# Kernel tuning notes

Hardware: AMD Instinct MI355X
Metric: run time of the kernel (lower is better)

Reference implementation:

```python
import jax, jax.numpy as jnp
import numpy as np

IN_C = 31
OUT_C = 31
GRID = 5          # grid_size
K = 3             # spline_order
NUM_BASIS = GRID + K                  # 8 B-spline basis functions
COEF_LEN = IN_C * OUT_C * NUM_BASIS   # 7688
UW_LEN = IN_C * OUT_C                 # 961 (univariate_weight)
RW_LEN = IN_C * OUT_C                 # 961 (residual_weight)
PNUM = COEF_LEN + UW_LEN + RW_LEN     # 9610 = kan_params_num


def _ext_grid():
    # uniform grid on grid_range=(-1,1), extended by K knots on each side
    h = 2.0 / GRID
    return jnp.arange(-K, GRID + K + 1, dtype=jnp.float32) * h - 1.0  # (GRID+2K+1,)


def bspline_basis(x):
    # x: (N, IN_C) -> (N, IN_C, NUM_BASIS) via Cox-de Boor recursion
    grid = _ext_grid()
    xx = x[..., None]
    b = ((xx >= grid[:-1]) & (xx < grid[1:])).astype(x.dtype)
    for p in range(1, K + 1):
        left = (xx - grid[: -(p + 1)]) / (grid[p:-1] - grid[: -(p + 1)]) * b[..., :-1]
        right = (grid[p + 1:] - xx) / (grid[p + 1:] - grid[1:-p]) * b[..., 1:]
        b = left + right
    return b


def setup_inputs() -> dict:
    key = jax.random.key(0)
    k1, k2, k3 = jax.random.split(key, 3)
    x = jax.random.normal(k1, (1, IN_C, 128, 128), jnp.float32)
    # HyperspectralGeneratorLayer: per-pixel (1x1 conv) map in_channels -> kan_params_num
    gen_w = jax.random.normal(k2, (PNUM, IN_C), jnp.float32) * 0.02
    gen_b = jax.random.normal(k3, (PNUM,), jnp.float32) * 0.02
    return {"x": x, "gen_w": gen_w, "gen_b": gen_b}


def reference(x, gen_w, gen_b):
    B, C, H, W = x.shape
    xf = x.transpose(0, 2, 3, 1).reshape(B * H * W, C)      # (N, 31)
    # generator: per-pixel KAN parameter vector (N, 9610)
    w = xf @ gen_w.T + gen_b
    coef = w[:, :COEF_LEN].reshape(-1, IN_C, OUT_C, NUM_BASIS)
    uw = w[:, COEF_LEN:COEF_LEN + UW_LEN].reshape(-1, IN_C, OUT_C)
    rw = w[:, COEF_LEN + UW_LEN:].reshape(-1, IN_C, OUT_C)
    # per-pixel KAN: phi_ij(x_i) = uw_ij * spline_ij(x_i) + rw_ij * silu(x_i); y_j = sum_i phi_ij
    basis = bspline_basis(xf)                               # (N, 31, 8)
    spline = jnp.einsum('nik,niok->nio', basis, coef)       # (N, 31, 31)
    y = jnp.einsum('nio,nio->no', spline, uw) \
        + jnp.einsum('ni,nio->no', jax.nn.silu(xf), rw)     # (N, 31)
    return y.reshape(B, H, W, OUT_C).transpose(0, 3, 1, 2)
```

## Files before the change

kernel.cpp:

```cpp
#include <hip/hip_runtime.h>
#include <hip/hip_bf16.h>
#include <math.h>

#define IN_C 31
#define OUT_C 31
#define NPIX 16384
#define UW_OFF 7688
#define RW_OFF 8649
#define PART_OFF (640 * 1024)
#define CHUNK_BYTES 20480

typedef __attribute__((ext_vector_type(8))) _Float16 f16x8;
typedef __attribute__((ext_vector_type(4))) float f32x4;

__device__ inline short f2h(float f) {
    union { _Float16 h; short s; } cv;
    cv.h = (_Float16)f;
    return cv.s;
}

__global__ __launch_bounds__(64) void kan_prep_kernel(
    const float* __restrict__ gw, const float* __restrict__ gb,
    unsigned short* __restrict__ ws)
{
    const int blk = blockIdx.x;
    const int i   = blk / 20;
    const int ch  = blk % 20;
    const int l   = threadIdx.x;
    const int col = l & 15;
    const int krow = l >> 4;
    const int o = (ch & 1) * 16 + col;

    int p;
    if (ch < 16)      p = (i * 31 + o) * 8 + (ch >> 1);
    else if (ch < 18) p = UW_OFF + i * 31 + o;
    else              p = RW_OFF + i * 31 + o;

    short v8[8];
#pragma unroll
    for (int j = 0; j < 8; ++j) {
        const int c = krow * 8 + j;
        float v = 0.f;
        if (o < OUT_C) v = (c < IN_C) ? gw[p * 31 + c] : gb[p];
        v8[j] = f2h(v);
    }
    *(f16x8*)&ws[(blk * 64 + l) * 8] = *(f16x8*)v8;
}

__device__ __forceinline__ void stage_i(const unsigned char* wsrc,
                                        unsigned char* ldst, int t) {
#pragma unroll
    for (int k = 0; k < 2; ++k) {
        const int off = (k * 512 + t) * 16;
        __builtin_amdgcn_global_load_lds(
            (const __attribute__((address_space(1))) unsigned int*)(wsrc + off),
            (__attribute__((address_space(3))) unsigned int*)(ldst + off),
            16, 0, 0);
    }
    if (t < 256) {
        const int off = (1024 + t) * 16;
        __builtin_amdgcn_global_load_lds(
            (const __attribute__((address_space(1))) unsigned int*)(wsrc + off),
            (__attribute__((address_space(3))) unsigned int*)(ldst + off),
            16, 0, 0);
    }
}

__device__ __forceinline__ void compute2(
    int iA, const unsigned char* wbA, bool hasB, int iB, const unsigned char* wbB,
    const float* __restrict__ x, int pr0, f16x8 xv8f, f32x4 Y[2], int l)
{
    const float xa = x[iA * NPIX + pr0];
    const float xb = hasB ? x[iB * NPIX + pr0] : 0.f;

    _Float16 basA[8], basB[8];
    f16x8 arwA, arwB;
#pragma unroll
    for (int s = 0; s < 2; ++s) {
        const float xv = (s == 0) ? xa : xb;
        const float tb = (xv + 2.2f) * 2.5f;
        const float jf = floorf(tb);
        const float u  = tb - jf;
        const int  jj  = (int)jf;
        const float u2 = u * u, u3 = u2 * u;
        const float b0v = u3 * (1.f / 6.f);
        const float b1v = (-3.f * u3 + 3.f * u2 + 3.f * u + 1.f) * (1.f / 6.f);
        const float b2v = (3.f * u3 - 6.f * u2 + 4.f) * (1.f / 6.f);
        const float omu = 1.f - u;
        const float b3v = omu * omu * omu * (1.f / 6.f);
#pragma unroll
        for (int m = 0; m < 8; ++m) {
            const int d = jj - m;
            const float bv = (d == 0) ? b0v : (d == 1) ? b1v : (d == 2) ? b2v
                           : (d == 3) ? b3v : 0.f;
            if (s == 0) basA[m] = (_Float16)bv; else basB[m] = (_Float16)bv;
        }
        const float sil = xv / (1.f + __expf(-xv));
        if (s == 0) arwA = xv8f * (_Float16)sil;
        else        arwB = xv8f * (_Float16)sil;
    }

    f32x4 SPA[2], UWA[2], SPB[2], UWB[2];
#pragma unroll
    for (int nt = 0; nt < 2; ++nt) {
        SPA[nt] = (f32x4){0.f, 0.f, 0.f, 0.f};
        UWA[nt] = (f32x4){0.f, 0.f, 0.f, 0.f};
        SPB[nt] = (f32x4){0.f, 0.f, 0.f, 0.f};
        UWB[nt] = (f32x4){0.f, 0.f, 0.f, 0.f};
    }

#pragma unroll
    for (int p = 0; p < 10; ++p) {
        const f16x8 a0 = *(const f16x8*)(wbA + ((p * 2 + 0) * 64 + l) * 16);
        const f16x8 a1 = *(const f16x8*)(wbA + ((p * 2 + 1) * 64 + l) * 16);
        const f16x8 c0 = *(const f16x8*)(wbB + ((p * 2 + 0) * 64 + l) * 16);
        const f16x8 c1 = *(const f16x8*)(wbB + ((p * 2 + 1) * 64 + l) * 16);
        if (p < 8) {
            const f16x8 afA = xv8f * basA[p];
            SPA[0] = __builtin_amdgcn_mfma_f32_16x16x32_f16(afA, a0, SPA[0], 0, 0, 0);
            SPA[1] = __builtin_amdgcn_mfma_f32_16x16x32_f16(afA, a1, SPA[1], 0, 0, 0);
            if (hasB) {
                const f16x8 afB = xv8f * basB[p];
                SPB[0] = __builtin_amdgcn_mfma_f32_16x16x32_f16(afB, c0, SPB[0], 0, 0, 0);
                SPB[1] = __builtin_amdgcn_mfma_f32_16x16x32_f16(afB, c1, SPB[1], 0, 0, 0);
            }
        } else if (p == 8) {
            UWA[0] = __builtin_amdgcn_mfma_f32_16x16x32_f16(xv8f, a0, UWA[0], 0, 0, 0);
            UWA[1] = __builtin_amdgcn_mfma_f32_16x16x32_f16(xv8f, a1, UWA[1], 0, 0, 0);
            if (hasB) {
                UWB[0] = __builtin_amdgcn_mfma_f32_16x16x32_f16(xv8f, c0, UWB[0], 0, 0, 0);
                UWB[1] = __builtin_amdgcn_mfma_f32_16x16x32_f16(xv8f, c1, UWB[1], 0, 0, 0);
            }
        } else {
            Y[0] = __builtin_amdgcn_mfma_f32_16x16x32_f16(arwA, a0, Y[0], 0, 0, 0);
            Y[1] = __builtin_amdgcn_mfma_f32_16x16x32_f16(arwA, a1, Y[1], 0, 0, 0);
            if (hasB) {
                Y[0] = __builtin_amdgcn_mfma_f32_16x16x32_f16(arwB, c0, Y[0], 0, 0, 0);
                Y[1] = __builtin_amdgcn_mfma_f32_16x16x32_f16(arwB, c1, Y[1], 0, 0, 0);
            }
        }
    }

#pragma unroll
    for (int nt = 0; nt < 2; ++nt)
#pragma unroll
        for (int r = 0; r < 4; ++r) {
            Y[nt][r] = fmaf(UWA[nt][r], SPA[nt][r], Y[nt][r]);
            if (hasB) Y[nt][r] = fmaf(UWB[nt][r], SPB[nt][r], Y[nt][r]);
        }
}

__global__ __launch_bounds__(512) void kan_mfma14_kernel(
    const float* __restrict__ x,
    const unsigned char* __restrict__ wsw,
    float* __restrict__ parts,
    float* __restrict__ out,
    int nsplit)
{
    const int t = threadIdx.x;
    const int l = t & 63;
    const int w = t >> 6;
    const int pix0 = blockIdx.x * 128;
    const int csize = (IN_C + nsplit - 1) / nsplit;
    const int ibase = blockIdx.y * csize;
    const int iend = min(ibase + csize, IN_C);

    __shared__ __align__(16) unsigned char bufs[2][CHUNK_BYTES];

    const int n0 = w * 16;
    const int pr0 = pix0 + n0 + (l & 15);

    stage_i(wsw + (size_t)ibase * CHUNK_BYTES, bufs[0], t);
    stage_i(wsw + (size_t)(ibase + 1) * CHUNK_BYTES, bufs[1], t);

    f16x8 xv8f;
    {
        const int cb = (l >> 4) * 8;
#pragma unroll
        for (int j = 0; j < 8; ++j) {
            const int c = cb + j;
            const float v = (c < IN_C) ? x[c * NPIX + pr0] : 1.0f;
            xv8f[j] = (_Float16)v;
        }
    }

    f32x4 Y[2];
    Y[0] = (f32x4){0.f, 0.f, 0.f, 0.f};
    Y[1] = (f32x4){0.f, 0.f, 0.f, 0.f};

    __syncthreads();

    compute2(ibase, bufs[0], true, ibase + 1, bufs[1], x, pr0, xv8f, Y, l);

    __syncthreads();

    const bool has3 = (ibase + 3) < iend;
    stage_i(wsw + (size_t)(ibase + 2) * CHUNK_BYTES, bufs[0], t);
    if (has3)
        stage_i(wsw + (size_t)(ibase + 3) * CHUNK_BYTES, bufs[1], t);

    __syncthreads();

    compute2(ibase + 2, bufs[0], has3, ibase + 3, bufs[1], x, pr0, xv8f, Y, l);

    __syncthreads();
    float* yb = (float*)bufs;
#pragma unroll
    for (int nt = 0; nt < 2; ++nt)
#pragma unroll
        for (int r = 0; r < 4; ++r) {
            const int p = n0 + (l >> 4) * 4 + r;
            const int o = nt * 16 + (l & 15);
            if (o < OUT_C) yb[p * 33 + o] = Y[nt][r];
        }
    __syncthreads();

    float* dst = (blockIdx.y == 0) ? out
               : (parts + (size_t)(blockIdx.y - 1) * OUT_C * NPIX);
    for (int idx = t; idx < 128 * OUT_C; idx += 512) {
        const int n = idx & 127, o = idx >> 7;
        dst[o * NPIX + pix0 + n] = yb[n * 33 + o];
    }
}

__global__ __launch_bounds__(256) void kan_combine_kernel(
    float* __restrict__ out, const float* __restrict__ parts, int npart)
{
    const int e = blockIdx.x * 256 + threadIdx.x;
    const int nv = (OUT_C * NPIX) / 4;
    if (e < nv) {
        f32x4 a = ((const f32x4*)out)[e];
        for (int j = 0; j < npart; ++j)
            a += ((const f32x4*)parts)[e + (size_t)j * nv];
        ((f32x4*)out)[e] = a;
    }
}

extern "C" void kernel_launch(void* const* d_in, const int* in_sizes, int n_in,
                              void* d_out, int out_size, void* d_ws, size_t ws_size,
                              hipStream_t stream) {
    const float* x  = (const float*)d_in[0];
    const float* gw = (const float*)d_in[1];
    const float* gb = (const float*)d_in[2];
    float* out = (float*)d_out;
    unsigned short* ws = (unsigned short*)d_ws;
    float* parts = (float*)((char*)d_ws + PART_OFF);

    const size_t part_bytes = (size_t)OUT_C * NPIX * 4;
    int nsplit = 8;
    if (ws_size < PART_OFF + 7 * part_bytes) nsplit = 4;
    if (ws_size < PART_OFF + 3 * part_bytes) nsplit = 2;

    hipLaunchKernelGGL(kan_prep_kernel, dim3(620), dim3(64), 0, stream, gw, gb, ws);
    hipLaunchKernelGGL(kan_mfma14_kernel, dim3(NPIX / 128, nsplit), dim3(512), 0, stream,
                       x, (const unsigned char*)d_ws, parts, out, nsplit);
    const int nv = (OUT_C * NPIX) / 4;
    hipLaunchKernelGGL(kan_combine_kernel, dim3((nv + 255) / 256), dim3(256), 0, stream,
                       out, parts, nsplit - 1);
}
```

Measured before the change: 41.99 us.

## Swap MFMA operands and apply spline basis weights after matmul in fp32

Instead of scaling the x vector by each basis value before each MFMA, the kernel now computes the plain generator product for each basis slot (weights as A, x as B) and applies the basis and silu weights in fp32 with FMA on the outputs. It also replaces the fixed two-pass structure with a generic loop over input-channel pairs, adding bounds checks. Each MFMA now starts from a zero accumulator followed by VALU FMAs, which removes the per-step f16 vector scaling but adds VALU work and serial dependencies. The output transpose indexing is changed to match the swapped operand layout.

```diff
diff --git a/kernel.cpp b/kernel.cpp
--- a/kernel.cpp
+++ b/kernel.cpp
@@ -66,91 +66,64 @@
     }
 }
 
-__device__ __forceinline__ void compute2(
-    int iA, const unsigned char* wbA, bool hasB, int iB, const unsigned char* wbB,
-    const float* __restrict__ x, int pr0, f16x8 xv8f, f32x4 Y[2], int l)
-{
-    const float xa = x[iA * NPIX + pr0];
-    const float xb = hasB ? x[iB * NPIX + pr0] : 0.f;
-
-    _Float16 basA[8], basB[8];
-    f16x8 arwA, arwB;
-#pragma unroll
-    for (int s = 0; s < 2; ++s) {
-        const float xv = (s == 0) ? xa : xb;
-        const float tb = (xv + 2.2f) * 2.5f;
-        const float jf = floorf(tb);
-        const float u  = tb - jf;
-        const int  jj  = (int)jf;
-        const float u2 = u * u, u3 = u2 * u;
-        const float b0v = u3 * (1.f / 6.f);
-        const float b1v = (-3.f * u3 + 3.f * u2 + 3.f * u + 1.f) * (1.f / 6.f);
-        const float b2v = (3.f * u3 - 6.f * u2 + 4.f) * (1.f / 6.f);
-        const float omu = 1.f - u;
-        const float b3v = omu * omu * omu * (1.f / 6.f);
-#pragma unroll
-        for (int m = 0; m < 8; ++m) {
-            const int d = jj - m;
-            const float bv = (d == 0) ? b0v : (d == 1) ? b1v : (d == 2) ? b2v
-                           : (d == 3) ? b3v : 0.f;
-            if (s == 0) basA[m] = (_Float16)bv; else basB[m] = (_Float16)bv;
-        }
-        const float sil = xv / (1.f + __expf(-xv));
-        if (s == 0) arwA = xv8f * (_Float16)sil;
-        else        arwB = xv8f * (_Float16)sil;
-    }
-
-    f32x4 SPA[2], UWA[2], SPB[2], UWB[2];
-#pragma unroll
-    for (int nt = 0; nt < 2; ++nt) {
-        SPA[nt] = (f32x4){0.f, 0.f, 0.f, 0.f};
-        UWA[nt] = (f32x4){0.f, 0.f, 0.f, 0.f};
-        SPB[nt] = (f32x4){0.f, 0.f, 0.f, 0.f};
-        UWB[nt] = (f32x4){0.f, 0.f, 0.f, 0.f};
-    }
-
-#pragma unroll
-    for (int p = 0; p < 10; ++p) {
-        const f16x8 a0 = *(const f16x8*)(wbA + ((p * 2 + 0) * 64 + l) * 16);
-        const f16x8 a1 = *(const f16x8*)(wbA + ((p * 2 + 1) * 64 + l) * 16);
-        const f16x8 c0 = *(const f16x8*)(wbB + ((p * 2 + 0) * 64 + l) * 16);
-        const f16x8 c1 = *(const f16x8*)(wbB + ((p * 2 + 1) * 64 + l) * 16);
-        if (p < 8) {
-            const f16x8 afA = xv8f * basA[p];
-            SPA[0] = __builtin_amdgcn_mfma_f32_16x16x32_f16(afA, a0, SPA[0], 0, 0, 0);
-            SPA[1] = __builtin_amdgcn_mfma_f32_16x16x32_f16(afA, a1, SPA[1], 0, 0, 0);
-            if (hasB) {
-                const f16x8 afB = xv8f * basB[p];
-                SPB[0] = __builtin_amdgcn_mfma_f32_16x16x32_f16(afB, c0, SPB[0], 0, 0, 0);
-                SPB[1] = __builtin_amdgcn_mfma_f32_16x16x32_f16(afB, c1, SPB[1], 0, 0, 0);
-            }
-        } else if (p == 8) {
-            UWA[0] = __builtin_amdgcn_mfma_f32_16x16x32_f16(xv8f, a0, UWA[0], 0, 0, 0);
-            UWA[1] = __builtin_amdgcn_mfma_f32_16x16x32_f16(xv8f, a1, UWA[1], 0, 0, 0);
-            if (hasB) {
-                UWB[0] = __builtin_amdgcn_mfma_f32_16x16x32_f16(xv8f, c0, UWB[0], 0, 0, 0);
-                UWB[1] = __builtin_amdgcn_mfma_f32_16x16x32_f16(xv8f, c1, UWB[1], 0, 0, 0);
-            }
-        } else {
-            Y[0] = __builtin_amdgcn_mfma_f32_16x16x32_f16(arwA, a0, Y[0], 0, 0, 0);
-            Y[1] = __builtin_amdgcn_mfma_f32_16x16x32_f16(arwA, a1, Y[1], 0, 0, 0);
-            if (hasB) {
-                Y[0] = __builtin_amdgcn_mfma_f32_16x16x32_f16(arwB, c0, Y[0], 0, 0, 0);
-                Y[1] = __builtin_amdgcn_mfma_f32_16x16x32_f16(arwB, c1, Y[1], 0, 0, 0);
-            }
-        }
-    }
-
-#pragma unroll
-    for (int nt = 0; nt < 2; ++nt)
+__device__ __forceinline__ void body_swap(
+    int i, const unsigned char* wb, const float* __restrict__ x, int pr0,
+    f16x8 ax, f32x4 Y[2], int l)
+{
+    const float xv = x[i * NPIX + pr0];
+
+    float bas[8];
+    const float tb = (xv + 2.2f) * 2.5f;
+    const float jf = floorf(tb);
+    const float u  = tb - jf;
+    const int  jj  = (int)jf;
+    const float u2 = u * u, u3 = u2 * u;
+    const float b0v = u3 * (1.f / 6.f);
+    const float b1v = (-3.f * u3 + 3.f * u2 + 3.f * u + 1.f) * (1.f / 6.f);
+    const float b2v = (3.f * u3 - 6.f * u2 + 4.f) * (1.f / 6.f);
+    const float omu = 1.f - u;
+    const float b3v = omu * omu * omu * (1.f / 6.f);
+#pragma unroll
+    for (int m = 0; m < 8; ++m) {
+        const int d = jj - m;
+        bas[m] = (d == 0) ? b0v : (d == 1) ? b1v : (d == 2) ? b2v
+               : (d == 3) ? b3v : 0.f;
+    }
+    const float sil = xv / (1.f + __expf(-xv));
+
+    const f32x4 z = (f32x4){0.f, 0.f, 0.f, 0.f};
+    f32x4 SP0 = z, SP1 = z;
+
+#pragma unroll
+    for (int p = 0; p < 8; ++p) {
+        const f16x8 a0 = *(const f16x8*)(wb + ((p * 2 + 0) * 64 + l) * 16);
+        const f16x8 a1 = *(const f16x8*)(wb + ((p * 2 + 1) * 64 + l) * 16);
+        const f32x4 T0 = __builtin_amdgcn_mfma_f32_16x16x32_f16(a0, ax, z, 0, 0, 0);
+        const f32x4 T1 = __builtin_amdgcn_mfma_f32_16x16x32_f16(a1, ax, z, 0, 0, 0);
 #pragma unroll
         for (int r = 0; r < 4; ++r) {
-            Y[nt][r] = fmaf(UWA[nt][r], SPA[nt][r], Y[nt][r]);
-            if (hasB) Y[nt][r] = fmaf(UWB[nt][r], SPB[nt][r], Y[nt][r]);
-        }
-}
-
-__global__ __launch_bounds__(512) void kan_mfma14_kernel(
+            SP0[r] = fmaf(bas[p], T0[r], SP0[r]);
+            SP1[r] = fmaf(bas[p], T1[r], SP1[r]);
+        }
+    }
+    {
+        const f16x8 u0 = *(const f16x8*)(wb + (16 * 64 + l) * 16);
+        const f16x8 u1 = *(const f16x8*)(wb + (17 * 64 + l) * 16);
+        const f16x8 r0 = *(const f16x8*)(wb + (18 * 64 + l) * 16);
+        const f16x8 r1 = *(const f16x8*)(wb + (19 * 64 + l) * 16);
+        const f32x4 UW0 = __builtin_amdgcn_mfma_f32_16x16x32_f16(u0, ax, z, 0, 0, 0);
+        const f32x4 UW1 = __builtin_amdgcn_mfma_f32_16x16x32_f16(u1, ax, z, 0, 0, 0);
+        const f32x4 R0  = __builtin_amdgcn_mfma_f32_16x16x32_f16(r0, ax, z, 0, 0, 0);
+        const f32x4 R1  = __builtin_amdgcn_mfma_f32_16x16x32_f16(r1, ax, z, 0, 0, 0);
+#pragma unroll
+        for (int r = 0; r < 4; ++r) {
+            Y[0][r] = fmaf(UW0[r], SP0[r], fmaf(sil, R0[r], Y[0][r]));
+            Y[1][r] = fmaf(UW1[r], SP1[r], fmaf(sil, R1[r], Y[1][r]));
+        }
+    }
+}
+
+__global__ __launch_bounds__(512) void kan_mfma15_kernel(
     const float* __restrict__ x,
     const unsigned char* __restrict__ wsw,
     float* __restrict__ parts,
@@ -167,20 +140,20 @@
 
     __shared__ __align__(16) unsigned char bufs[2][CHUNK_BYTES];
 
-    const int n0 = w * 16;
-    const int pr0 = pix0 + n0 + (l & 15);
+    const int pr0 = pix0 + w * 16 + (l & 15);
 
     stage_i(wsw + (size_t)ibase * CHUNK_BYTES, bufs[0], t);
-    stage_i(wsw + (size_t)(ibase + 1) * CHUNK_BYTES, bufs[1], t);
-
-    f16x8 xv8f;
+    if (ibase + 1 < iend)
+        stage_i(wsw + (size_t)(ibase + 1) * CHUNK_BYTES, bufs[1], t);
+
+    f16x8 ax;
     {
         const int cb = (l >> 4) * 8;
 #pragma unroll
         for (int j = 0; j < 8; ++j) {
             const int c = cb + j;
             const float v = (c < IN_C) ? x[c * NPIX + pr0] : 1.0f;
-            xv8f[j] = (_Float16)v;
+            ax[j] = (_Float16)v;
         }
     }
 
@@ -190,27 +163,27 @@
 
     __syncthreads();
 
-    compute2(ibase, bufs[0], true, ibase + 1, bufs[1], x, pr0, xv8f, Y, l);
-
-    __syncthreads();
-
-    const bool has3 = (ibase + 3) < iend;
-    stage_i(wsw + (size_t)(ibase + 2) * CHUNK_BYTES, bufs[0], t);
-    if (has3)
-        stage_i(wsw + (size_t)(ibase + 3) * CHUNK_BYTES, bufs[1], t);
-
-    __syncthreads();
-
-    compute2(ibase + 2, bufs[0], has3, ibase + 3, bufs[1], x, pr0, xv8f, Y, l);
-
-    __syncthreads();
+#pragma unroll 1
+    for (int i0 = ibase; i0 < iend; i0 += 2) {
+        if (i0 > ibase) {
+            stage_i(wsw + (size_t)i0 * CHUNK_BYTES, bufs[0], t);
+            if (i0 + 1 < iend)
+                stage_i(wsw + (size_t)(i0 + 1) * CHUNK_BYTES, bufs[1], t);
+            __syncthreads();
+        }
+        body_swap(i0, bufs[0], x, pr0, ax, Y, l);
+        if (i0 + 1 < iend)
+            body_swap(i0 + 1, bufs[1], x, pr0, ax, Y, l);
+        __syncthreads();
+    }
+
     float* yb = (float*)bufs;
 #pragma unroll
     for (int nt = 0; nt < 2; ++nt)
 #pragma unroll
         for (int r = 0; r < 4; ++r) {
-            const int p = n0 + (l >> 4) * 4 + r;
-            const int o = nt * 16 + (l & 15);
+            const int o = nt * 16 + (l >> 4) * 4 + r;
+            const int p = w * 16 + (l & 15);
             if (o < OUT_C) yb[p * 33 + o] = Y[nt][r];
         }
     __syncthreads();
@@ -252,7 +225,7 @@
     if (ws_size < PART_OFF + 3 * part_bytes) nsplit = 2;
 
     hipLaunchKernelGGL(kan_prep_kernel, dim3(620), dim3(64), 0, stream, gw, gb, ws);
-    hipLaunchKernelGGL(kan_mfma14_kernel, dim3(NPIX / 128, nsplit), dim3(512), 0, stream,
+    hipLaunchKernelGGL(kan_mfma15_kernel, dim3(NPIX / 128, nsplit), dim3(512), 0, stream,
                        x, (const unsigned char*)d_ws, parts, out, nsplit);
     const int nv = (OUT_C * NPIX) / 4;
     hipLaunchKernelGGL(kan_combine_kernel, dim3((nv + 255) / 256), dim3(256), 0, stream,
```

After: 41.90 us. Within noise of the previous version (-0.2%).
